# Kernel tuning notes

Measured on AMD Instinct MI355X. Metric: run time of the kernel, lower is better.

Reference implementation:

```python
import jax, jax.numpy as jnp
import numpy as np

B, S, D, H, DK = 8, 1024, 768, 12, 64


def setup_inputs() -> dict:
    key = jax.random.key(0)
    k1, k2, k3, k4, k5 = jax.random.split(key, 5)
    return {
        "x": jax.random.normal(k1, (B, S, D), dtype=jnp.float32),
        "Wq": jax.random.normal(k2, (H, D, DK), dtype=jnp.float32),
        "Wk": jax.random.normal(k3, (H, D, DK), dtype=jnp.float32),
        "Wv": jax.random.normal(k4, (H, D, DK), dtype=jnp.float32),
        "W": jax.random.normal(k5, (D, D), dtype=jnp.float32),
    }


def reference(x, Wq, Wk, Wv, W):
    # Batched equivalent of the per-head SelfAttention loop + concat + W matmul.
    q = jnp.einsum("bsd,hdk->bhsk", x, Wq)  # [B,H,S,DK]
    k = jnp.einsum("bsd,hdk->bhsk", x, Wk)
    v = jnp.einsum("bsd,hdk->bhsk", x, Wv)
    scale = 1.0 / jnp.sqrt(jnp.asarray(DK, dtype=x.dtype))
    scores = jnp.einsum("bhsk,bhtk->bhst", q, k) * scale  # [B,H,S,S]
    attn = jax.nn.softmax(scores, axis=-1)
    z = jnp.einsum("bhst,bhtk->bhsk", attn, v)  # [B,H,S,DK]
    # concat heads along last dim: [B,S,H*DK]
    z = jnp.transpose(z, (0, 2, 1, 3)).reshape(x.shape[0], x.shape[1], H * DK)
    return jnp.matmul(z, W)  # [B,S,D]
```

## Files before the change

### kernel.cpp

```cpp
#include <hip/hip_runtime.h>

#define Bv 8
#define Sv 1024
#define Dv 768
#define Hv 12
#define DKv 64
#define Mv (Bv*Sv)
#define NQKV (3*Hv*DKv)
#define NQK (2*Hv*DKv)

typedef __attribute__((ext_vector_type(8))) short short8;
typedef __attribute__((ext_vector_type(4))) float f32x4;

__device__ __forceinline__ short f2bf(float f) {
    unsigned u = __builtin_bit_cast(unsigned, f);
    u += 0x7fffu + ((u >> 16) & 1u);
    return (short)(u >> 16);
}
__device__ __forceinline__ float bf2f(short h) {
    return __builtin_bit_cast(float, (unsigned)(unsigned short)h << 16);
}

__device__ __forceinline__ f32x4 mfma16(short8 a, short8 b, f32x4 c) {
    return __builtin_amdgcn_mfma_f32_16x16x32_bf16(a, b, c, 0, 0, 0);
}

__device__ __forceinline__ void gload16(const short* g, const short* l) {
    __builtin_amdgcn_global_load_lds(
        (const __attribute__((address_space(1))) unsigned int*)g,
        (__attribute__((address_space(3))) unsigned int*)(short*)l, 16, 0, 0);
}

__global__ void split_x_kernel(const float* __restrict__ x, short* __restrict__ xh,
                               short* __restrict__ xl) {
    int t = blockIdx.x * 256 + threadIdx.x;
    const float4* f = (const float4*)x + (size_t)t * 2;
    float4 a = f[0], b = f[1];
    float v[8] = {a.x,a.y,a.z,a.w,b.x,b.y,b.z,b.w};
    short8 oh, ol;
#pragma unroll
    for (int k = 0; k < 8; k++) {
        short hi = f2bf(v[k]);
        oh[k] = hi;
        ol[k] = f2bf(v[k] - bf2f(hi));
    }
    *((short8*)xh + t) = oh;
    *((short8*)xl + t) = ol;
}

__global__ void pack_wqkv_kernel(const float* __restrict__ Wq, const float* __restrict__ Wk,
                                 const float* __restrict__ Wv, short* __restrict__ Wh,
                                 short* __restrict__ Wl) {
    int dt = blockIdx.x;
    int h  = blockIdx.y;
    int p  = blockIdx.z;
    const float* S = (p == 0 ? Wq : (p == 1 ? Wk : Wv)) + (size_t)h * Dv * DKv;
    float sc = (p == 0) ? 0.125f : 1.0f;
    __shared__ float lds[64][65];
    int t = threadIdx.x;
    int d0 = dt * 64;
#pragma unroll
    for (int i = 0; i < 4; i++) {
        int v = t + i * 256;
        int r = v >> 4, c4 = v & 15;
        float4 f = *(const float4*)&S[(size_t)(d0 + r) * DKv + c4 * 4];
        lds[r][c4*4+0] = f.x; lds[r][c4*4+1] = f.y; lds[r][c4*4+2] = f.z; lds[r][c4*4+3] = f.w;
    }
    __syncthreads();
#pragma unroll
    for (int i = 0; i < 2; i++) {
        int v = t + i * 256;
        int kk = v >> 3, dl0 = (v & 7) * 8;
        short8 oh, ol;
#pragma unroll
        for (int k = 0; k < 8; k++) {
            float f = lds[dl0 + k][kk] * sc;
            short hi = f2bf(f);
            oh[k] = hi;
            ol[k] = f2bf(f - bf2f(hi));
        }
        size_t base = (size_t)(p*768 + h*64 + kk) * Dv + d0 + dl0;
        *(short8*)&Wh[base] = oh;
        if (p < 2) *(short8*)&Wl[base] = ol;
    }
}

__global__ void transpose_cast_kernel(const float* __restrict__ S, int S_cols,
                                      short* __restrict__ D, int D_ld) {
    int c0 = blockIdx.x * 64, r0 = blockIdx.y * 64;
    __shared__ float lds[64][65];
    int t = threadIdx.x;
#pragma unroll
    for (int i = 0; i < 4; i++) {
        int v = t + i * 256;
        int r = v >> 4, c4 = v & 15;
        float4 f = *(const float4*)&S[(size_t)(r0 + r) * S_cols + c0 + c4 * 4];
        lds[r][c4*4+0] = f.x; lds[r][c4*4+1] = f.y; lds[r][c4*4+2] = f.z; lds[r][c4*4+3] = f.w;
    }
    __syncthreads();
#pragma unroll
    for (int i = 0; i < 2; i++) {
        int v = t + i * 256;
        int oc = v >> 3, rl0 = (v & 7) * 8;
        short8 o;
#pragma unroll
        for (int k = 0; k < 8; k++) o[k] = f2bf(lds[rl0 + k][oc]);
        *(short8*)&D[(size_t)(c0 + oc) * D_ld + r0 + rl0] = o;
    }
}

__global__ void vtrans_kernel(const short* __restrict__ QKVh, short* __restrict__ Vt) {
    int sc = blockIdx.x;
    int bh = blockIdx.y;
    int b = bh / Hv, h = bh % Hv;
    __shared__ __align__(16) short lds[64][72];
    int t = threadIdx.x;
    int s0 = sc * 64;
#pragma unroll
    for (int i = 0; i < 2; i++) {
        int v = t + i * 256;
        int sl = v >> 3, c0 = (v & 7) * 8;
        short8 xv = *(const short8*)&QKVh[(size_t)(b*Sv + s0 + sl) * NQKV + NQK + h*DKv + c0];
        *(short8*)&lds[sl][c0] = xv;
    }
    __syncthreads();
#pragma unroll
    for (int i = 0; i < 2; i++) {
        int v = t + i * 256;
        int dk = v >> 3, tl0 = (v & 7) * 8;
        short8 o;
#pragma unroll
        for (int k = 0; k < 8; k++) o[k] = lds[tl0 + k][dk];
        *(short8*)&Vt[(size_t)(bh*64 + dk) * Sv + s0 + tl0] = o;
    }
}

__device__ __forceinline__ void swz_xy(int n, int& xbl, int& ybl) {
    int cx = n & 7, k = n >> 3;
    ybl = cx + 8 * (k & 7);
    xbl = k >> 3;
}

__global__ __launch_bounds__(256, 4) void gemm1_kernel(const short* __restrict__ xh,
                                                       const short* __restrict__ xl,
                                                       const short* __restrict__ Wh,
                                                       const short* __restrict__ Wl,
                                                       short* __restrict__ QKVh,
                                                       short* __restrict__ QKVl) {
    int xbl, ybl;
    swz_xy(blockIdx.x, xbl, ybl);
    int m0 = ybl * 128, n0 = xbl * 128;
    bool isv = (n0 >= NQK);
    int KT = isv ? 24 : 72;
    __shared__ __align__(16) short lA[2][4096];
    __shared__ __align__(16) short lB[2][4096];
    int tid = threadIdx.x, lane = tid & 63, w = tid >> 6;
    int wr = w >> 1, wc = w & 1;
    int li = lane & 15, g = lane >> 4;
    f32x4 zero = {0.f, 0.f, 0.f, 0.f};
    f32x4 acc[4][4];
#pragma unroll
    for (int i = 0; i < 4; i++)
#pragma unroll
        for (int j = 0; j < 4; j++) acc[i][j] = zero;

    int e0 = tid * 8;
    int sr0 = e0 >> 5;
    int sc0 = ((e0 >> 3) & 3) ^ ((sr0 >> 1) & 3);
    int sr1 = sr0 + 64;
    int sc1 = ((e0 >> 3) & 3) ^ ((sr1 >> 1) & 3);

    auto stage = [&](int t, int buf) {
        int seg = (t >= 48) ? 2 : (t >= 24 ? 1 : 0);
        int kk = (t - seg * 24) * 32;
        const short* Ab = (seg == 2) ? xl : xh;
        const short* Bb = (seg == 1) ? Wl : Wh;
        gload16(Ab + (size_t)(m0 + sr0) * Dv + kk + sc0 * 8, &lA[buf][w * 512]);
        gload16(Bb + (size_t)(n0 + sr0) * Dv + kk + sc0 * 8, &lB[buf][w * 512]);
        gload16(Ab + (size_t)(m0 + sr1) * Dv + kk + sc1 * 8, &lA[buf][2048 + w * 512]);
        gload16(Bb + (size_t)(n0 + sr1) * Dv + kk + sc1 * 8, &lB[buf][2048 + w * 512]);
    };

    stage(0, 0);
    asm volatile("s_waitcnt vmcnt(0)" ::: "memory");
    __builtin_amdgcn_s_barrier();

    for (int t = 0; t < KT; t++) {
        int cur = t & 1;
        if (t + 1 < KT) stage(t + 1, cur ^ 1);
        __builtin_amdgcn_sched_barrier(0);
        short8 a[4], bb[4];
#pragma unroll
        for (int mi = 0; mi < 4; mi++) {
            int row = wr*64 + mi*16 + li;
            a[mi] = *(const short8*)&lA[cur][row * 32 + ((g ^ ((row >> 1) & 3)) << 3)];
        }
#pragma unroll
        for (int ni = 0; ni < 4; ni++) {
            int row = wc*64 + ni*16 + li;
            bb[ni] = *(const short8*)&lB[cur][row * 32 + ((g ^ ((row >> 1) & 3)) << 3)];
        }
#pragma unroll
        for (int mi = 0; mi < 4; mi++)
#pragma unroll
            for (int ni = 0; ni < 4; ni++)
                acc[mi][ni] = mfma16(a[mi], bb[ni], acc[mi][ni]);
        asm volatile("s_waitcnt vmcnt(0)" ::: "memory");
        __builtin_amdgcn_s_barrier();
        __builtin_amdgcn_sched_barrier(0);
    }
#pragma unroll
    for (int mi = 0; mi < 4; mi++)
#pragma unroll
        for (int ni = 0; ni < 4; ni++)
#pragma unroll
            for (int j = 0; j < 4; j++) {
                int row = m0 + wr*64 + mi*16 + g*4 + j;
                int col = n0 + wc*64 + ni*16 + li;
                float v = acc[mi][ni][j];
                short hi = f2bf(v);
                QKVh[(size_t)row * NQKV + col] = hi;
                if (!isv) QKVl[(size_t)row * NQK + col] = f2bf(v - bf2f(hi));
            }
}

__global__ __launch_bounds__(256, 4) void gemm2_kernel(const short* __restrict__ A,
                                                       const short* __restrict__ Bt,
                                                       float* __restrict__ C) {
    int xbl, ybl;
    swz_xy(blockIdx.x, xbl, ybl);
    int m0 = ybl * 128, n0 = xbl * 128;
    __shared__ __align__(16) short lA[2][4096];
    __shared__ __align__(16) short lB[2][4096];
    int tid = threadIdx.x, lane = tid & 63, w = tid >> 6;
    int wr = w >> 1, wc = w & 1;
    int li = lane & 15, g = lane >> 4;
    f32x4 zero = {0.f, 0.f, 0.f, 0.f};
    f32x4 acc[4][4];
#pragma unroll
    for (int i = 0; i < 4; i++)
#pragma unroll
        for (int j = 0; j < 4; j++) acc[i][j] = zero;

    int e0 = tid * 8;
    int sr0 = e0 >> 5;
    int sc0 = ((e0 >> 3) & 3) ^ ((sr0 >> 1) & 3);
    int sr1 = sr0 + 64;
    int sc1 = ((e0 >> 3) & 3) ^ ((sr1 >> 1) & 3);

    auto stage = [&](int t, int buf) {
        int kk = t * 32;
        gload16(A  + (size_t)(m0 + sr0) * Dv + kk + sc0 * 8, &lA[buf][w * 512]);
        gload16(Bt + (size_t)(n0 + sr0) * Dv + kk + sc0 * 8, &lB[buf][w * 512]);
        gload16(A  + (size_t)(m0 + sr1) * Dv + kk + sc1 * 8, &lA[buf][2048 + w * 512]);
        gload16(Bt + (size_t)(n0 + sr1) * Dv + kk + sc1 * 8, &lB[buf][2048 + w * 512]);
    };

    stage(0, 0);
    asm volatile("s_waitcnt vmcnt(0)" ::: "memory");
    __builtin_amdgcn_s_barrier();

    for (int t = 0; t < 24; t++) {
        int cur = t & 1;
        if (t + 1 < 24) stage(t + 1, cur ^ 1);
        __builtin_amdgcn_sched_barrier(0);
        short8 a[4], bb[4];
#pragma unroll
        for (int mi = 0; mi < 4; mi++) {
            int row = wr*64 + mi*16 + li;
            a[mi] = *(const short8*)&lA[cur][row * 32 + ((g ^ ((row >> 1) & 3)) << 3)];
        }
#pragma unroll
        for (int ni = 0; ni < 4; ni++) {
            int row = wc*64 + ni*16 + li;
            bb[ni] = *(const short8*)&lB[cur][row * 32 + ((g ^ ((row >> 1) & 3)) << 3)];
        }
#pragma unroll
        for (int mi = 0; mi < 4; mi++)
#pragma unroll
            for (int ni = 0; ni < 4; ni++)
                acc[mi][ni] = mfma16(a[mi], bb[ni], acc[mi][ni]);
        asm volatile("s_waitcnt vmcnt(0)" ::: "memory");
        __builtin_amdgcn_s_barrier();
        __builtin_amdgcn_sched_barrier(0);
    }
#pragma unroll
    for (int mi = 0; mi < 4; mi++)
#pragma unroll
        for (int ni = 0; ni < 4; ni++)
#pragma unroll
            for (int j = 0; j < 4; j++) {
                int row = m0 + wr*64 + mi*16 + g*4 + j;
                int col = n0 + wc*64 + ni*16 + li;
                C[(size_t)row * Dv + col] = acc[mi][ni][j];
            }
}

__global__ __launch_bounds__(512, 6) void attn_kernel(const short* __restrict__ QKVh,
                                                      const short* __restrict__ QKVl,
                                                      const short* __restrict__ Vt,
                                                      short* __restrict__ Z) {
    int n = blockIdx.x;
    int j2 = n >> 3;
    int bh = (n & 7) + 8 * (j2 >> 3);
    int qb = j2 & 7;
    int b = bh / Hv, h = bh % Hv;
    int tid = threadIdx.x, lane = tid & 63, w = tid >> 6;
    int li = lane & 15, g = lane >> 4;

    __shared__ __align__(16) short Kh[64 * 64];
    __shared__ __align__(16) short Kl[64 * 64];
    __shared__ __align__(16) short Vs[64 * 64];
    __shared__ __align__(16) short P[8][1024];
    char* Pw = (char*)&P[w][0];
    const char* Khc = (const char*)Kh;
    const char* Klc = (const char*)Kl;
    const char* Vsc = (const char*)Vs;

    int qr0 = qb * 128 + w * 16;
    const short* qhr = QKVh + (size_t)(b*Sv + qr0 + li) * NQKV + h * DKv;
    const short* qlr = QKVl + (size_t)(b*Sv + qr0 + li) * NQK  + h * DKv;
    short8 qh0 = *(const short8*)(qhr + g * 8);
    short8 qh1 = *(const short8*)(qhr + 32 + g * 8);
    short8 ql0 = *(const short8*)(qlr + g * 8);
    short8 ql1 = *(const short8*)(qlr + 32 + g * 8);

    const short* Khb = QKVh + (size_t)(b*Sv) * NQKV + Hv*DKv + h*DKv;
    const short* Klb = QKVl + (size_t)(b*Sv) * NQK  + Hv*DKv + h*DKv;
    const short* Vbase = Vt + (size_t)(bh * 64) * Sv;

    int srow = w * 8 + (lane >> 3);
    int scs  = (lane & 7) ^ (srow & 7);

    float mm = -1e30f, ll = 0.f;
    f32x4 zero = {0.f, 0.f, 0.f, 0.f};
    f32x4 acc[4];
#pragma unroll
    for (int ni = 0; ni < 4; ni++) acc[ni] = zero;

    for (int t = 0; t < 16; t++) {
        int t0 = t * 64;
        gload16(Khb + (size_t)(t0 + srow) * NQKV + scs * 8, &Kh[w * 512]);
        gload16(Klb + (size_t)(t0 + srow) * NQK  + scs * 8, &Kl[w * 512]);
        gload16(Vbase + (size_t)srow * Sv + t0 + scs * 8,   &Vs[w * 512]);
        __syncthreads();

        f32x4 s[4];
#pragma unroll
        for (int tn = 0; tn < 4; tn++) {
            int row = tn * 16 + li;
            int rb = row * 128, rs = (row & 7) << 4;
            short8 kh0 = *(const short8*)(Khc + rb + ((g << 4) ^ rs));
            short8 kh1 = *(const short8*)(Khc + rb + ((64 + (g << 4)) ^ rs));
            short8 kl0 = *(const short8*)(Klc + rb + ((g << 4) ^ rs));
            short8 kl1 = *(const short8*)(Klc + rb + ((64 + (g << 4)) ^ rs));
            f32x4 z = mfma16(kh0, qh0, zero);
            z = mfma16(kh1, qh1, z);
            z = mfma16(kl0, qh0, z);
            z = mfma16(kl1, qh1, z);
            z = mfma16(kh0, ql0, z);
            z = mfma16(kh1, ql1, z);
            s[tn] = z;
        }
        float rm = s[0][0];
#pragma unroll
        for (int tn = 0; tn < 4; tn++)
#pragma unroll
            for (int jj = 0; jj < 4; jj++) rm = fmaxf(rm, s[tn][jj]);
        rm = fmaxf(rm, __shfl_xor(rm, 16));
        rm = fmaxf(rm, __shfl_xor(rm, 32));
        float mn = fmaxf(mm, rm);
        float sfu = __expf(mm - mn);
        float p[4][4];
        float rs2 = 0.f;
#pragma unroll
        for (int tn = 0; tn < 4; tn++)
#pragma unroll
            for (int jj = 0; jj < 4; jj++) { p[tn][jj] = __expf(s[tn][jj] - mn); rs2 += p[tn][jj]; }
        rs2 += __shfl_xor(rs2, 16);
        rs2 += __shfl_xor(rs2, 32);
        ll = ll * sfu + rs2;
        mm = mn;

        float sfq[4];
#pragma unroll
        for (int jj = 0; jj < 4; jj++) sfq[jj] = __shfl(sfu, g * 4 + jj);
#pragma unroll
        for (int ni = 0; ni < 4; ni++)
#pragma unroll
            for (int jj = 0; jj < 4; jj++) acc[ni][jj] *= sfq[jj];

#pragma unroll
        for (int tn = 0; tn < 4; tn++) {
            unsigned lo, hi;
            asm("v_cvt_pk_bf16_f32 %0, %1, %2" : "=v"(lo) : "v"(p[tn][0]), "v"(p[tn][1]));
            asm("v_cvt_pk_bf16_f32 %0, %1, %2" : "=v"(hi) : "v"(p[tn][2]), "v"(p[tn][3]));
            unsigned long long pk = (unsigned long long)lo | ((unsigned long long)hi << 32);
            int off = (li * 128 + tn * 32 + g * 8) ^ ((li & 7) << 4);
            *(unsigned long long*)(Pw + off) = pk;
        }
#pragma unroll
        for (int kt = 0; kt < 2; kt++) {
            int roff = (li * 128 + kt * 64 + g * 16) ^ ((li & 7) << 4);
            short8 ap = *(const short8*)(Pw + roff);
#pragma unroll
            for (int ni = 0; ni < 4; ni++) {
                int dk = ni * 16 + li;
                int vb = dk * 128 + ((((kt * 4 + g) << 4)) ^ ((dk & 7) << 4));
                short8 bv = *(const short8*)(Vsc + vb);
                acc[ni] = mfma16(ap, bv, acc[ni]);
            }
        }
        __syncthreads();
    }
    float inv = 1.f / ll;
    float invq[4];
#pragma unroll
    for (int jj = 0; jj < 4; jj++) invq[jj] = __shfl(inv, g * 4 + jj);
#pragma unroll
    for (int ni = 0; ni < 4; ni++)
#pragma unroll
        for (int jj = 0; jj < 4; jj++) {
            int row = b*Sv + qr0 + g*4 + jj;
            int col = h*DKv + ni*16 + li;
            Z[(size_t)row * Dv + col] = f2bf(acc[ni][jj] * invq[jj]);
        }
}

extern "C" void kernel_launch(void* const* d_in, const int* in_sizes, int n_in,
                              void* d_out, int out_size, void* d_ws, size_t ws_size,
                              hipStream_t stream) {
    const float* x  = (const float*)d_in[0];
    const float* Wq = (const float*)d_in[1];
    const float* Wk = (const float*)d_in[2];
    const float* Wv = (const float*)d_in[3];
    const float* W  = (const float*)d_in[4];
    float* out = (float*)d_out;

    short* xh   = (short*)d_ws;
    short* xl   = xh   + (size_t)Mv * Dv;
    short* Wh   = xl   + (size_t)Mv * Dv;
    short* Wl   = Wh   + (size_t)NQKV * Dv;
    short* W2T  = Wl   + (size_t)NQKV * Dv;
    short* QKVh = W2T  + (size_t)Dv * Dv;
    short* QKVl = QKVh + (size_t)Mv * NQKV;
    short* Vt   = QKVl + (size_t)Mv * NQK;
    short* Zb   = Vt   + (size_t)Bv*Hv*DKv * Sv;

    split_x_kernel<<<dim3(Mv * Dv / (256 * 8)), 256, 0, stream>>>(x, xh, xl);
    pack_wqkv_kernel<<<dim3(Dv/64, Hv, 3), 256, 0, stream>>>(Wq, Wk, Wv, Wh, Wl);
    transpose_cast_kernel<<<dim3(Dv/64, Dv/64), 256, 0, stream>>>(W, Dv, W2T, Dv);
    gemm1_kernel<<<dim3((NQKV/128) * (Mv/128)), 256, 0, stream>>>(xh, xl, Wh, Wl, QKVh, QKVl);
    vtrans_kernel<<<dim3(Sv/64, Bv*Hv), 256, 0, stream>>>(QKVh, Vt);
    attn_kernel<<<dim3(768), 512, 0, stream>>>(QKVh, QKVl, Vt, Zb);
    gemm2_kernel<<<dim3((Dv/128) * (Mv/128)), 256, 0, stream>>>(Zb, W2T, out);
}
```

Before: 202.6 us.

## Triple-buffer LDS staging in projection GEMMs with two-tile prefetch

```diff
diff --git a/kernel.cpp b/kernel.cpp
--- a/kernel.cpp
+++ b/kernel.cpp
@@ -152,8 +152,8 @@
     int m0 = ybl * 128, n0 = xbl * 128;
     bool isv = (n0 >= NQK);
     int KT = isv ? 24 : 72;
-    __shared__ __align__(16) short lA[2][4096];
-    __shared__ __align__(16) short lB[2][4096];
+    __shared__ __align__(16) short lA[3][4096];
+    __shared__ __align__(16) short lB[3][4096];
     int tid = threadIdx.x, lane = tid & 63, w = tid >> 6;
     int wr = w >> 1, wc = w & 1;
     int li = lane & 15, g = lane >> 4;
@@ -182,12 +182,18 @@
     };
 
     stage(0, 0);
-    asm volatile("s_waitcnt vmcnt(0)" ::: "memory");
-    __builtin_amdgcn_s_barrier();
-
+    stage(1, 1);
+
+    int cur = 0;
     for (int t = 0; t < KT; t++) {
-        int cur = t & 1;
-        if (t + 1 < KT) stage(t + 1, cur ^ 1);
+        if (t + 1 < KT) asm volatile("s_waitcnt vmcnt(4)" ::: "memory");
+        else            asm volatile("s_waitcnt vmcnt(0)" ::: "memory");
+        __builtin_amdgcn_s_barrier();
+        __builtin_amdgcn_sched_barrier(0);
+        if (t + 2 < KT) {
+            int nb = cur + 2; if (nb >= 3) nb -= 3;
+            stage(t + 2, nb);
+        }
         __builtin_amdgcn_sched_barrier(0);
         short8 a[4], bb[4];
 #pragma unroll
@@ -205,9 +211,8 @@
 #pragma unroll
             for (int ni = 0; ni < 4; ni++)
                 acc[mi][ni] = mfma16(a[mi], bb[ni], acc[mi][ni]);
-        asm volatile("s_waitcnt vmcnt(0)" ::: "memory");
-        __builtin_amdgcn_s_barrier();
-        __builtin_amdgcn_sched_barrier(0);
+        __builtin_amdgcn_sched_barrier(0);
+        cur = (cur + 1 == 3) ? 0 : cur + 1;
     }
 #pragma unroll
     for (int mi = 0; mi < 4; mi++)
@@ -230,8 +235,8 @@
     int xbl, ybl;
     swz_xy(blockIdx.x, xbl, ybl);
     int m0 = ybl * 128, n0 = xbl * 128;
-    __shared__ __align__(16) short lA[2][4096];
-    __shared__ __align__(16) short lB[2][4096];
+    __shared__ __align__(16) short lA[3][4096];
+    __shared__ __align__(16) short lB[3][4096];
     int tid = threadIdx.x, lane = tid & 63, w = tid >> 6;
     int wr = w >> 1, wc = w & 1;
     int li = lane & 15, g = lane >> 4;
@@ -257,12 +262,18 @@
     };
 
     stage(0, 0);
-    asm volatile("s_waitcnt vmcnt(0)" ::: "memory");
-    __builtin_amdgcn_s_barrier();
-
+    stage(1, 1);
+
+    int cur = 0;
     for (int t = 0; t < 24; t++) {
-        int cur = t & 1;
-        if (t + 1 < 24) stage(t + 1, cur ^ 1);
+        if (t + 1 < 24) asm volatile("s_waitcnt vmcnt(4)" ::: "memory");
+        else            asm volatile("s_waitcnt vmcnt(0)" ::: "memory");
+        __builtin_amdgcn_s_barrier();
+        __builtin_amdgcn_sched_barrier(0);
+        if (t + 2 < 24) {
+            int nb = cur + 2; if (nb >= 3) nb -= 3;
+            stage(t + 2, nb);
+        }
         __builtin_amdgcn_sched_barrier(0);
         short8 a[4], bb[4];
 #pragma unroll
@@ -280,9 +291,8 @@
 #pragma unroll
             for (int ni = 0; ni < 4; ni++)
                 acc[mi][ni] = mfma16(a[mi], bb[ni], acc[mi][ni]);
-        asm volatile("s_waitcnt vmcnt(0)" ::: "memory");
-        __builtin_amdgcn_s_barrier();
-        __builtin_amdgcn_sched_barrier(0);
+        __builtin_amdgcn_sched_barrier(0);
+        cur = (cur + 1 == 3) ? 0 : cur + 1;
     }
 #pragma unroll
     for (int mi = 0; mi < 4; mi++)
```

Result: no change. 205.7 us (+1.5%).

## Enlarge QKV projection GEMM tiles to 256x256 with 512 threads

Applied to the files above, without the earlier changes.

```diff
diff --git a/kernel.cpp b/kernel.cpp
--- a/kernel.cpp
+++ b/kernel.cpp
@@ -141,82 +141,94 @@
     xbl = k >> 3;
 }
 
-__global__ __launch_bounds__(256, 4) void gemm1_kernel(const short* __restrict__ xh,
+__global__ __launch_bounds__(512, 2) void gemm1_kernel(const short* __restrict__ xh,
                                                        const short* __restrict__ xl,
                                                        const short* __restrict__ Wh,
                                                        const short* __restrict__ Wl,
                                                        short* __restrict__ QKVh,
                                                        short* __restrict__ QKVl) {
-    int xbl, ybl;
-    swz_xy(blockIdx.x, xbl, ybl);
-    int m0 = ybl * 128, n0 = xbl * 128;
+    int wgid = (blockIdx.x & 7) * 36 + (blockIdx.x >> 3);
+    int nt = wgid >> 5, mt = wgid & 31;
+    int m0 = mt * 256, n0 = nt * 256;
     bool isv = (n0 >= NQK);
-    int KT = isv ? 24 : 72;
-    __shared__ __align__(16) short lA[2][4096];
-    __shared__ __align__(16) short lB[2][4096];
+    int KT = isv ? 12 : 36;
+
+    __shared__ __align__(16) short lA[2][16384];
+    __shared__ __align__(16) short lB[2][16384];
     int tid = threadIdx.x, lane = tid & 63, w = tid >> 6;
-    int wr = w >> 1, wc = w & 1;
+    int wr = w >> 2, wcn = w & 3;
     int li = lane & 15, g = lane >> 4;
+
     f32x4 zero = {0.f, 0.f, 0.f, 0.f};
-    f32x4 acc[4][4];
-#pragma unroll
-    for (int i = 0; i < 4; i++)
+    f32x4 acc[8][4];
+#pragma unroll
+    for (int i = 0; i < 8; i++)
 #pragma unroll
         for (int j = 0; j < 4; j++) acc[i][j] = zero;
 
-    int e0 = tid * 8;
-    int sr0 = e0 >> 5;
-    int sc0 = ((e0 >> 3) & 3) ^ ((sr0 >> 1) & 3);
-    int sr1 = sr0 + 64;
-    int sc1 = ((e0 >> 3) & 3) ^ ((sr1 >> 1) & 3);
-
-    auto stage = [&](int t, int buf) {
-        int seg = (t >= 48) ? 2 : (t >= 24 ? 1 : 0);
-        int kk = (t - seg * 24) * 32;
+    int srow[4], scol[4];
+#pragma unroll
+    for (int i = 0; i < 4; i++) {
+        int r = i * 64 + (tid >> 3);
+        srow[i] = r;
+        scol[i] = ((tid & 7) ^ (r & 7)) << 3;
+    }
+
+    auto stage = [&](int kt, int buf) {
+        int seg = kt / 12;
+        int kk = (kt - seg * 12) * 64;
         const short* Ab = (seg == 2) ? xl : xh;
         const short* Bb = (seg == 1) ? Wl : Wh;
-        gload16(Ab + (size_t)(m0 + sr0) * Dv + kk + sc0 * 8, &lA[buf][w * 512]);
-        gload16(Bb + (size_t)(n0 + sr0) * Dv + kk + sc0 * 8, &lB[buf][w * 512]);
-        gload16(Ab + (size_t)(m0 + sr1) * Dv + kk + sc1 * 8, &lA[buf][2048 + w * 512]);
-        gload16(Bb + (size_t)(n0 + sr1) * Dv + kk + sc1 * 8, &lB[buf][2048 + w * 512]);
+#pragma unroll
+        for (int i = 0; i < 4; i++)
+            gload16(Ab + (size_t)(m0 + srow[i]) * Dv + kk + scol[i], &lA[buf][i * 4096 + w * 512]);
+#pragma unroll
+        for (int i = 0; i < 4; i++)
+            gload16(Bb + (size_t)(n0 + srow[i]) * Dv + kk + scol[i], &lB[buf][i * 4096 + w * 512]);
     };
 
     stage(0, 0);
     asm volatile("s_waitcnt vmcnt(0)" ::: "memory");
     __builtin_amdgcn_s_barrier();
 
-    for (int t = 0; t < KT; t++) {
-        int cur = t & 1;
-        if (t + 1 < KT) stage(t + 1, cur ^ 1);
+    for (int kt = 0; kt < KT; kt++) {
+        int buf = kt & 1;
+        if (kt + 1 < KT) stage(kt + 1, buf ^ 1);
         __builtin_amdgcn_sched_barrier(0);
-        short8 a[4], bb[4];
-#pragma unroll
-        for (int mi = 0; mi < 4; mi++) {
-            int row = wr*64 + mi*16 + li;
-            a[mi] = *(const short8*)&lA[cur][row * 32 + ((g ^ ((row >> 1) & 3)) << 3)];
-        }
-#pragma unroll
-        for (int ni = 0; ni < 4; ni++) {
-            int row = wc*64 + ni*16 + li;
-            bb[ni] = *(const short8*)&lB[cur][row * 32 + ((g ^ ((row >> 1) & 3)) << 3)];
-        }
-#pragma unroll
-        for (int mi = 0; mi < 4; mi++)
-#pragma unroll
-            for (int ni = 0; ni < 4; ni++)
-                acc[mi][ni] = mfma16(a[mi], bb[ni], acc[mi][ni]);
+#pragma unroll
+        for (int ks = 0; ks < 2; ks++) {
+            short8 a[8], b[4];
+#pragma unroll
+            for (int mi = 0; mi < 8; mi++) {
+                int r = wr * 128 + mi * 16 + li;
+                a[mi] = *(const short8*)&lA[buf][r * 64 + (((ks * 4 + g) ^ (r & 7)) << 3)];
+            }
+#pragma unroll
+            for (int ni = 0; ni < 4; ni++) {
+                int r = wcn * 64 + ni * 16 + li;
+                b[ni] = *(const short8*)&lB[buf][r * 64 + (((ks * 4 + g) ^ (r & 7)) << 3)];
+            }
+            __builtin_amdgcn_s_setprio(1);
+#pragma unroll
+            for (int mi = 0; mi < 8; mi++)
+#pragma unroll
+                for (int ni = 0; ni < 4; ni++)
+                    acc[mi][ni] = mfma16(a[mi], b[ni], acc[mi][ni]);
+            __builtin_amdgcn_s_setprio(0);
+        }
         asm volatile("s_waitcnt vmcnt(0)" ::: "memory");
         __builtin_amdgcn_s_barrier();
         __builtin_amdgcn_sched_barrier(0);
     }
-#pragma unroll
-    for (int mi = 0; mi < 4; mi++)
+
+#pragma unroll
+    for (int mi = 0; mi < 8; mi++)
 #pragma unroll
         for (int ni = 0; ni < 4; ni++)
 #pragma unroll
             for (int j = 0; j < 4; j++) {
-                int row = m0 + wr*64 + mi*16 + g*4 + j;
-                int col = n0 + wc*64 + ni*16 + li;
+                int row = m0 + wr * 128 + mi * 16 + g * 4 + j;
+                int col = n0 + wcn * 64 + ni * 16 + li;
                 float v = acc[mi][ni][j];
                 short hi = f2bf(v);
                 QKVh[(size_t)row * NQKV + col] = hi;
@@ -450,7 +462,7 @@
     split_x_kernel<<<dim3(Mv * Dv / (256 * 8)), 256, 0, stream>>>(x, xh, xl);
     pack_wqkv_kernel<<<dim3(Dv/64, Hv, 3), 256, 0, stream>>>(Wq, Wk, Wv, Wh, Wl);
     transpose_cast_kernel<<<dim3(Dv/64, Dv/64), 256, 0, stream>>>(W, Dv, W2T, Dv);
-    gemm1_kernel<<<dim3((NQKV/128) * (Mv/128)), 256, 0, stream>>>(xh, xl, Wh, Wl, QKVh, QKVl);
+    gemm1_kernel<<<dim3((NQKV/256) * (Mv/256)), 512, 0, stream>>>(xh, xl, Wh, Wl, QKVh, QKVl);
     vtrans_kernel<<<dim3(Sv/64, Bv*Hv), 256, 0, stream>>>(QKVh, Vt);
     attn_kernel<<<dim3(768), 512, 0, stream>>>(QKVh, QKVl, Vt, Zb);
     gemm2_kernel<<<dim3((Dv/128) * (Mv/128)), 256, 0, stream>>>(Zb, W2T, out);
```

After: 277.8 us. 37.1% more time.
